# Kernel tuning notes

Measured on AMD Instinct MI355X. Metric: run time of the kernel, lower is better.

The kernel has to match this reference:

```python
import jax, jax.numpy as jnp
import numpy as np

BS, SEQ, H, L = 2, 4096, 768, 8921

def setup_inputs() -> dict:
    key = jax.random.key(0)
    k1, k2, k3 = jax.random.split(key, 3)
    return {
        "code_features": jax.random.normal(k1, (L, H), dtype=jnp.float32),
        "text_features": jax.random.normal(k2, (BS, SEQ, H), dtype=jnp.float32),
        "attention_mask": jnp.ones((BS, SEQ), dtype=jnp.int32),
        "W": jax.random.normal(k3, (H, H), dtype=jnp.float32) * (1.0 / np.sqrt(H)),
    }

def reference(code_features, text_features, attention_mask, W):
    # projected = tanh(Linear(text)) : (bs, seq, h)
    projected = jnp.tanh(jnp.einsum("bsh,kh->bsk", text_features, W))
    # scores: (bs, seq, labels); code_features broadcasts over batch
    scores = jnp.einsum("bsh,lh->bsl", projected, code_features)
    # softmax over the SEQ axis (dim=1), then transpose -> (bs, labels, seq)
    att_weights = jnp.transpose(jax.nn.softmax(scores, axis=1), (0, 2, 1))
    # weighted sum over seq -> (bs, labels, h)
    weighted_output = jnp.einsum("bls,bsh->blh", att_weights, text_features)
    return (att_weights, weighted_output)
```

## Files before the change

kernel.cpp:

```cpp
#include <hip/hip_runtime.h>
#include <math.h>

#define BSZ  2
#define SEQN 4096
#define HD   768
#define NL   8921

typedef _Float16 f16;
typedef f16   f16x8 __attribute__((ext_vector_type(8)));
typedef float f32x4 __attribute__((ext_vector_type(4)));

#define GPTR(p) ((const __attribute__((address_space(1))) void*)(p))
#define LPTR(p) ((__attribute__((address_space(3))) void*)(p))

__device__ __forceinline__ void stage_region(const f16* __restrict__ src, int ldk,
                                             int row0, int rowMax, int kbase,
                                             f16* region, int t)
{
    const int lane = t & 63, wv = t >> 6;
    #pragma unroll
    for (int qq = 0; qq < 2; ++qq) {
        const int base16 = wv * 64 + qq * 512;
        const int off16  = base16 + lane;
        const int row    = off16 >> 2;
        const int chunk  = off16 & 3;
        const int schunk = chunk ^ ((row >> 1) & 3);
        int grow = row0 + row; if (grow > rowMax) grow = rowMax;
        const f16* g = src + (long long)grow * ldk + kbase + schunk * 8;
        __builtin_amdgcn_global_load_lds(GPTR(g), LPTR(region + base16 * 8), 16, 0, 0);
    }
}

#define PH_SYNC_ENTER()                                          \
    __builtin_amdgcn_sched_barrier(0);                           \
    __builtin_amdgcn_s_barrier();                                \
    asm volatile("s_waitcnt lgkmcnt(0)" ::: "memory");           \
    __builtin_amdgcn_sched_barrier(0);                           \
    __builtin_amdgcn_s_setprio(1);

#define PH_SYNC_EXIT()                                           \
    __builtin_amdgcn_s_setprio(0);                               \
    __builtin_amdgcn_sched_barrier(0);                           \
    __builtin_amdgcn_s_barrier();

__global__ __launch_bounds__(512, 2)
void gemm8p(const f16* __restrict__ A, const f16* __restrict__ B,
            float* __restrict__ C, int M, int N, int K,
            long long sA, long long sB, long long sC, int ldA, int ldB)
{
    __shared__ __align__(16) f16 SH[2][2][2][256 * 32];

    const int t    = threadIdx.x;
    const int lane = t & 63;
    const int wv   = t >> 6;
    const int wm   = wv >> 2;
    const int wn   = wv & 3;
    const int rl   = lane & 15;
    const int swz8 = (((lane >> 4) ^ ((rl >> 1) & 3)) * 8);

    const int nx = gridDim.x, nwg = nx * gridDim.y;
    {
    }
    int orig = blockIdx.y * nx + blockIdx.x;
    const int q = nwg >> 3, r = nwg & 7, xcd = orig & 7, sub = orig >> 3;
    const int wg = (xcd < r ? xcd * (q + 1) : r * (q + 1) + (xcd - r) * q) + sub;
    const int bx = wg % nx, by = wg / nx;

    const f16* Ab = A + (long long)blockIdx.z * sA;
    const f16* Bb = B + (long long)blockIdx.z * sB;
    float*     Cb = C + (long long)blockIdx.z * sC;

    const int m0 = by * 256, n0 = bx * 256;
    const int NT = K >> 6;
    const int Mm1 = M - 1, Nm1 = N - 1;

    f32x4 acc[8][4];
    #pragma unroll
    for (int i = 0; i < 8; ++i)
        #pragma unroll
        for (int j = 0; j < 4; ++j)
            acc[i][j] = (f32x4)0.f;

    stage_region(Ab, ldA, m0, Mm1, 0,  &SH[0][0][0][0], t);
    stage_region(Bb, ldB, n0, Nm1, 0,  &SH[0][1][0][0], t);
    stage_region(Ab, ldA, m0, Mm1, 32, &SH[0][0][1][0], t);
    stage_region(Bb, ldB, n0, Nm1, 32, &SH[0][1][1][0], t);
    stage_region(Ab, ldA, m0, Mm1, 64, &SH[1][0][0][0], t);
    stage_region(Bb, ldB, n0, Nm1, 64, &SH[1][1][0][0], t);
    stage_region(Ab, ldA, m0, Mm1, 96, &SH[1][0][1][0], t);
    asm volatile("s_waitcnt vmcnt(6)" ::: "memory");
    __builtin_amdgcn_sched_barrier(0);
    __builtin_amdgcn_s_barrier();

    for (int tt = 0; tt < NT; ++tt) {
        const int buf = tt & 1;
        const f16* As0 = &SH[buf][0][0][0];
        const f16* As1 = &SH[buf][0][1][0];
        const f16* Bs0 = &SH[buf][1][0][0];
        const f16* Bs1 = &SH[buf][1][1][0];

        f16x8 af[8], bfa, bfb, bfc, bfd;

        #pragma unroll
        for (int f = 0; f < 8; ++f)
            af[f] = *(const f16x8*)&As0[(wm * 128 + f * 16 + rl) * 32 + swz8];
        bfa = *(const f16x8*)&Bs0[(wn * 64 + 0 * 16 + rl) * 32 + swz8];
        bfb = *(const f16x8*)&Bs0[(wn * 64 + 1 * 16 + rl) * 32 + swz8];
        if (tt + 1 < NT)
            stage_region(Bb, ldB, n0, Nm1, (tt + 1) * 64 + 32, &SH[buf ^ 1][1][1][0], t);
        PH_SYNC_ENTER();
        #pragma unroll
        for (int f = 0; f < 8; ++f) {
            acc[f][0] = __builtin_amdgcn_mfma_f32_16x16x32_f16(af[f], bfa, acc[f][0], 0, 0, 0);
            acc[f][1] = __builtin_amdgcn_mfma_f32_16x16x32_f16(af[f], bfb, acc[f][1], 0, 0, 0);
        }
        PH_SYNC_EXIT();

        bfc = *(const f16x8*)&Bs0[(wn * 64 + 2 * 16 + rl) * 32 + swz8];
        bfd = *(const f16x8*)&Bs0[(wn * 64 + 3 * 16 + rl) * 32 + swz8];
        if (tt + 2 < NT)
            stage_region(Ab, ldA, m0, Mm1, (tt + 2) * 64, &SH[buf][0][0][0], t);
        PH_SYNC_ENTER();
        #pragma unroll
        for (int f = 0; f < 8; ++f) {
            acc[f][2] = __builtin_amdgcn_mfma_f32_16x16x32_f16(af[f], bfc, acc[f][2], 0, 0, 0);
            acc[f][3] = __builtin_amdgcn_mfma_f32_16x16x32_f16(af[f], bfd, acc[f][3], 0, 0, 0);
        }
        PH_SYNC_EXIT();

        #pragma unroll
        for (int f = 0; f < 8; ++f)
            af[f] = *(const f16x8*)&As1[(wm * 128 + f * 16 + rl) * 32 + swz8];
        bfa = *(const f16x8*)&Bs1[(wn * 64 + 0 * 16 + rl) * 32 + swz8];
        bfb = *(const f16x8*)&Bs1[(wn * 64 + 1 * 16 + rl) * 32 + swz8];
        if (tt + 2 < NT)
            stage_region(Bb, ldB, n0, Nm1, (tt + 2) * 64, &SH[buf][1][0][0], t);
        PH_SYNC_ENTER();
        #pragma unroll
        for (int f = 0; f < 8; ++f) {
            acc[f][0] = __builtin_amdgcn_mfma_f32_16x16x32_f16(af[f], bfa, acc[f][0], 0, 0, 0);
            acc[f][1] = __builtin_amdgcn_mfma_f32_16x16x32_f16(af[f], bfb, acc[f][1], 0, 0, 0);
        }
        PH_SYNC_EXIT();

        bfc = *(const f16x8*)&Bs1[(wn * 64 + 2 * 16 + rl) * 32 + swz8];
        bfd = *(const f16x8*)&Bs1[(wn * 64 + 3 * 16 + rl) * 32 + swz8];
        if (tt + 2 < NT)
            stage_region(Ab, ldA, m0, Mm1, (tt + 2) * 64 + 32, &SH[buf][0][1][0], t);
        __builtin_amdgcn_sched_barrier(0);
        __builtin_amdgcn_s_barrier();
        asm volatile("s_waitcnt lgkmcnt(0)" ::: "memory");
        __builtin_amdgcn_sched_barrier(0);
        __builtin_amdgcn_s_setprio(1);
        #pragma unroll
        for (int f = 0; f < 8; ++f) {
            acc[f][2] = __builtin_amdgcn_mfma_f32_16x16x32_f16(af[f], bfc, acc[f][2], 0, 0, 0);
            acc[f][3] = __builtin_amdgcn_mfma_f32_16x16x32_f16(af[f], bfd, acc[f][3], 0, 0, 0);
        }
        __builtin_amdgcn_s_setprio(0);
        asm volatile("s_waitcnt vmcnt(6)" ::: "memory");
        __builtin_amdgcn_sched_barrier(0);
        __builtin_amdgcn_s_barrier();
    }

    const int rq = (lane >> 4) * 4;
    #pragma unroll
    for (int f = 0; f < 8; ++f) {
        #pragma unroll
        for (int j = 0; j < 4; ++j) {
            #pragma unroll
            for (int rr = 0; rr < 4; ++rr) {
                const int row = m0 + wm * 128 + f * 16 + rq + rr;
                const int col = n0 + wn * 64 + j * 16 + rl;
                if (row < M)
                    Cb[(long long)row * N + col] = acc[f][j][rr];
            }
        }
    }
}

template<int S16>
__device__ inline void stage_tile(const void* srcv, int ldk, int row0, int rowMax,
                                  int kt, f16* dst, int t, int lane, int wv)
{
    if constexpr (S16) {
        const f16* src = (const f16*)srcv;
        #pragma unroll
        for (int j = 0; j < 2; ++j) {
            int r = wv * 32 + j * 16 + (lane >> 2);
            int row = row0 + r; if (row > rowMax) row = rowMax;
            const f16* g = src + (long long)row * ldk + kt + (lane & 3) * 8;
            f16* l = dst + (wv * 32 + j * 16) * 32;
            __builtin_amdgcn_global_load_lds(GPTR(g), LPTR(l), 16, 0, 0);
        }
    } else {
        const float* src = (const float*)srcv;
        int r  = t >> 1;
        int kq = (t & 1) * 16;
        int row = row0 + r; if (row > rowMax) row = rowMax;
        const float* g = src + (long long)row * ldk + kt + kq;
        float4 v0 = ((const float4*)g)[0];
        float4 v1 = ((const float4*)g)[1];
        float4 v2 = ((const float4*)g)[2];
        float4 v3 = ((const float4*)g)[3];
        f16x8 h0, h1;
        h0[0]=(f16)v0.x; h0[1]=(f16)v0.y; h0[2]=(f16)v0.z; h0[3]=(f16)v0.w;
        h0[4]=(f16)v1.x; h0[5]=(f16)v1.y; h0[6]=(f16)v1.z; h0[7]=(f16)v1.w;
        h1[0]=(f16)v2.x; h1[1]=(f16)v2.y; h1[2]=(f16)v2.z; h1[3]=(f16)v2.w;
        h1[4]=(f16)v3.x; h1[5]=(f16)v3.y; h1[6]=(f16)v3.z; h1[7]=(f16)v3.w;
        *(f16x8*)&dst[r * 32 + kq]     = h0;
        *(f16x8*)&dst[r * 32 + kq + 8] = h1;
    }
}

template<int SA, int SB, int OUTMODE>
__global__ __launch_bounds__(256)
void mfma_nt(const void* __restrict__ A, const void* __restrict__ B,
             void* __restrict__ C, int M, int N, int K,
             long long sA, long long sB, long long sC, int ldA, int ldB)
{
    const char* Ab = (const char*)A + (long long)blockIdx.z * sA * (SA ? 2 : 4);
    const char* Bb = (const char*)B + (long long)blockIdx.z * sB * (SB ? 2 : 4);

    __shared__ __align__(16) f16 As[128 * 32];
    __shared__ __align__(16) f16 Bs[128 * 32];

    const int t    = threadIdx.x;
    const int lane = t & 63;
    const int wv   = t >> 6;
    const int wr   = wv >> 1;
    const int wc   = wv & 1;
    const int m0   = blockIdx.y * 128;
    const int n0   = blockIdx.x * 128;

    f32x4 acc[4][4] = {};

    for (int kt = 0; kt < K; kt += 32) {
        stage_tile<SA>(Ab, ldA, m0, M - 1, kt, As, t, lane, wv);
        stage_tile<SB>(Bb, ldB, n0, N - 1, kt, Bs, t, lane, wv);
        __syncthreads();

        f16x8 af[4], bf[4];
        const int kc = (lane >> 4) * 8;
        const int rl = lane & 15;
        #pragma unroll
        for (int i = 0; i < 4; ++i)
            af[i] = *(const f16x8*)&As[(wr * 64 + i * 16 + rl) * 32 + kc];
        #pragma unroll
        for (int j = 0; j < 4; ++j)
            bf[j] = *(const f16x8*)&Bs[(wc * 64 + j * 16 + rl) * 32 + kc];

        #pragma unroll
        for (int i = 0; i < 4; ++i)
            #pragma unroll
            for (int j = 0; j < 4; ++j)
                acc[i][j] = __builtin_amdgcn_mfma_f32_16x16x32_f16(af[i], bf[j], acc[i][j], 0, 0, 0);
        __syncthreads();
    }

    const int rquad = (lane >> 4) * 4;
    const int rcol  = lane & 15;
    #pragma unroll
    for (int i = 0; i < 4; ++i) {
        #pragma unroll
        for (int j = 0; j < 4; ++j) {
            #pragma unroll
            for (int r = 0; r < 4; ++r) {
                int row = m0 + wr * 64 + i * 16 + rquad + r;
                int col = n0 + wc * 64 + j * 16 + rcol;
                if (row < M) {
                    if constexpr (OUTMODE == 1)
                        ((f16*)C)[(long long)row * N + col] = (f16)tanhf(acc[i][j][r]);
                    else
                        ((float*)C + (long long)blockIdx.z * sC)[(long long)row * N + col] = acc[i][j][r];
                }
            }
        }
    }
}

__global__ __launch_bounds__(256)
void cvt_f32_f16(const float* __restrict__ in, f16* __restrict__ out, long long n4)
{
    long long i = (long long)blockIdx.x * 256 + threadIdx.x;
    if (i < n4) {
        float4 v = ((const float4*)in)[i];
        f16 h[4] = {(f16)v.x, (f16)v.y, (f16)v.z, (f16)v.w};
        *(uint2*)&out[i * 4] = *(uint2*)h;
    }
}

__global__ __launch_bounds__(256)
void transpose_f16(const float* __restrict__ in, f16* __restrict__ out)
{
    __shared__ float tile[32][33];
    const int b  = blockIdx.z;
    const int h0 = blockIdx.x * 32, s0 = blockIdx.y * 32;
    in  += (long long)b * SEQN * HD;
    out += (long long)b * HD * SEQN;
    const int tx = threadIdx.x & 31, ty = threadIdx.x >> 5;
    #pragma unroll
    for (int i = ty; i < 32; i += 8)
        tile[i][tx] = in[(long long)(s0 + i) * HD + h0 + tx];
    __syncthreads();
    #pragma unroll
    for (int i = ty; i < 32; i += 8)
        out[(long long)(h0 + i) * SEQN + s0 + tx] = (f16)tile[tx][i];
}

template<bool W16>
__global__ __launch_bounds__(256)
void softmax_rows(float* __restrict__ data, f16* __restrict__ data16)
{
    const long long row = blockIdx.x;
    float* p = data + row * (long long)SEQN;
    const int t = threadIdx.x;

    float4 v[4];
    float vmax = -INFINITY;
    #pragma unroll
    for (int i = 0; i < 4; ++i) {
        v[i] = ((const float4*)p)[t + 256 * i];
        vmax = fmaxf(vmax, fmaxf(fmaxf(v[i].x, v[i].y), fmaxf(v[i].z, v[i].w)));
    }
    #pragma unroll
    for (int off = 32; off > 0; off >>= 1)
        vmax = fmaxf(vmax, __shfl_xor(vmax, off));

    __shared__ float redmax[4];
    __shared__ float redsum[4];
    if ((t & 63) == 0) redmax[t >> 6] = vmax;
    __syncthreads();
    vmax = fmaxf(fmaxf(redmax[0], redmax[1]), fmaxf(redmax[2], redmax[3]));

    float sum = 0.f;
    #pragma unroll
    for (int i = 0; i < 4; ++i) {
        v[i].x = expf(v[i].x - vmax);
        v[i].y = expf(v[i].y - vmax);
        v[i].z = expf(v[i].z - vmax);
        v[i].w = expf(v[i].w - vmax);
        sum += (v[i].x + v[i].y) + (v[i].z + v[i].w);
    }
    #pragma unroll
    for (int off = 32; off > 0; off >>= 1)
        sum += __shfl_xor(sum, off);
    if ((t & 63) == 0) redsum[t >> 6] = sum;
    __syncthreads();
    sum = (redsum[0] + redsum[1]) + (redsum[2] + redsum[3]);

    const float inv = 1.0f / sum;
    #pragma unroll
    for (int i = 0; i < 4; ++i) {
        v[i].x *= inv; v[i].y *= inv; v[i].z *= inv; v[i].w *= inv;
        ((float4*)p)[t + 256 * i] = v[i];
        if constexpr (W16) {
            f16 h[4] = {(f16)v[i].x, (f16)v[i].y, (f16)v[i].z, (f16)v[i].w};
            *(uint2*)&data16[row * (long long)SEQN + (t + 256 * i) * 4] = *(uint2*)h;
        }
    }
}

#define BMF 64
#define BNF 64
#define BKF 16
#define PADF 4

template<bool TANH>
__global__ __launch_bounds__(256)
void nt_gemm(const float* __restrict__ A, const float* __restrict__ B,
             float* __restrict__ C, int M, int N, int K,
             long long sA, long long sB, long long sC)
{
    A += (long long)blockIdx.z * sA;
    B += (long long)blockIdx.z * sB;
    C += (long long)blockIdx.z * sC;
    __shared__ __align__(16) float As[BKF][BMF + PADF];
    __shared__ __align__(16) float Bs[BKF][BNF + PADF];
    const int t = threadIdx.x;
    const int m0 = blockIdx.y * BMF, n0 = blockIdx.x * BNF;
    const int tx = t & 15, ty = t >> 4, lr = t >> 2, lk = (t & 3) * 4;
    float acc[4][4] = {};
    for (int kt = 0; kt < K; kt += BKF) {
        {
            float4 v = make_float4(0.f, 0.f, 0.f, 0.f);
            int m = m0 + lr;
            if (m < M) v = *(const float4*)(A + (long long)m * K + kt + lk);
            As[lk+0][lr]=v.x; As[lk+1][lr]=v.y; As[lk+2][lr]=v.z; As[lk+3][lr]=v.w;
        }
        {
            float4 v = make_float4(0.f, 0.f, 0.f, 0.f);
            int n = n0 + lr;
            if (n < N) v = *(const float4*)(B + (long long)n * K + kt + lk);
            Bs[lk+0][lr]=v.x; Bs[lk+1][lr]=v.y; Bs[lk+2][lr]=v.z; Bs[lk+3][lr]=v.w;
        }
        __syncthreads();
        #pragma unroll
        for (int k = 0; k < BKF; ++k) {
            float4 a = *(const float4*)(&As[k][ty * 4]);
            float4 b = *(const float4*)(&Bs[k][tx * 4]);
            float av[4]={a.x,a.y,a.z,a.w}, bv[4]={b.x,b.y,b.z,b.w};
            #pragma unroll
            for (int i = 0; i < 4; ++i)
                #pragma unroll
                for (int j = 0; j < 4; ++j)
                    acc[i][j] = fmaf(av[i], bv[j], acc[i][j]);
        }
        __syncthreads();
    }
    #pragma unroll
    for (int i = 0; i < 4; ++i) {
        int m = m0 + ty * 4 + i;
        if (m < M) {
            float4 r;
            r.x = TANH ? tanhf(acc[i][0]) : acc[i][0];
            r.y = TANH ? tanhf(acc[i][1]) : acc[i][1];
            r.z = TANH ? tanhf(acc[i][2]) : acc[i][2];
            r.w = TANH ? tanhf(acc[i][3]) : acc[i][3];
            *(float4*)(C + (long long)m * N + n0 + tx * 4) = r;
        }
    }
}

__global__ __launch_bounds__(256)
void nn_gemm(const float* __restrict__ A, const float* __restrict__ B,
             float* __restrict__ C, int M, int N, int K,
             long long sA, long long sB, long long sC)
{
    A += (long long)blockIdx.z * sA;
    B += (long long)blockIdx.z * sB;
    C += (long long)blockIdx.z * sC;
    __shared__ __align__(16) float As[BKF][BMF + PADF];
    __shared__ __align__(16) float Bs[BKF][BNF + PADF];
    const int t = threadIdx.x;
    const int m0 = blockIdx.y * BMF, n0 = blockIdx.x * BNF;
    const int tx = t & 15, ty = t >> 4, lr = t >> 2, lk = (t & 3) * 4;
    const int kr = t >> 4, cq = (t & 15) * 4;
    float acc[4][4] = {};
    for (int kt = 0; kt < K; kt += BKF) {
        {
            float4 v = make_float4(0.f, 0.f, 0.f, 0.f);
            int m = m0 + lr;
            if (m < M) v = *(const float4*)(A + (long long)m * K + kt + lk);
            As[lk+0][lr]=v.x; As[lk+1][lr]=v.y; As[lk+2][lr]=v.z; As[lk+3][lr]=v.w;
        }
        {
            float4 v = *(const float4*)(B + (long long)(kt + kr) * N + n0 + cq);
            *(float4*)(&Bs[kr][cq]) = v;
        }
        __syncthreads();
        #pragma unroll
        for (int k = 0; k < BKF; ++k) {
            float4 a = *(const float4*)(&As[k][ty * 4]);
            float4 b = *(const float4*)(&Bs[k][tx * 4]);
            float av[4]={a.x,a.y,a.z,a.w}, bv[4]={b.x,b.y,b.z,b.w};
            #pragma unroll
            for (int i = 0; i < 4; ++i)
                #pragma unroll
                for (int j = 0; j < 4; ++j)
                    acc[i][j] = fmaf(av[i], bv[j], acc[i][j]);
        }
        __syncthreads();
    }
    #pragma unroll
    for (int i = 0; i < 4; ++i) {
        int m = m0 + ty * 4 + i;
        if (m < M)
            *(float4*)(C + (long long)m * N + n0 + tx * 4) =
                make_float4(acc[i][0], acc[i][1], acc[i][2], acc[i][3]);
    }
}

extern "C" void kernel_launch(void* const* d_in, const int* in_sizes, int n_in,
                              void* d_out, int out_size, void* d_ws, size_t ws_size,
                              hipStream_t stream)
{
    const float* code = (const float*)d_in[0];
    const float* text = (const float*)d_in[1];
    const float* Wm   = (const float*)d_in[3];

    float* att  = (float*)d_out;
    float* wout = att + (long long)BSZ * NL * SEQN;

    const long long n_code  = (long long)NL * HD;
    const long long n_proj  = (long long)BSZ * SEQN * HD;
    const long long n_textT = (long long)BSZ * HD * SEQN;
    const long long n_att   = (long long)BSZ * NL * SEQN;
    const size_t base_bytes = (size_t)(n_code + n_proj + n_textT) * 2;
    const size_t full_bytes = base_bytes + (size_t)n_att * 2;

    if (ws_size < base_bytes) {
        float* proj = wout;
        dim3 g1(HD / BNF, (BSZ * SEQN) / BMF, 1);
        hipLaunchKernelGGL((nt_gemm<true>), g1, dim3(256), 0, stream,
                           text, Wm, proj, BSZ * SEQN, HD, HD, 0LL, 0LL, 0LL);
        dim3 g2(SEQN / BNF, (NL + BMF - 1) / BMF, BSZ);
        hipLaunchKernelGGL((nt_gemm<false>), g2, dim3(256), 0, stream,
                           code, proj, att, NL, SEQN, HD,
                           0LL, (long long)SEQN * HD, (long long)NL * SEQN);
        hipLaunchKernelGGL((softmax_rows<false>), dim3(BSZ * NL), dim3(256), 0, stream, att, (f16*)nullptr);
        dim3 g4(HD / BNF, (NL + BMF - 1) / BMF, BSZ);
        hipLaunchKernelGGL(nn_gemm, g4, dim3(256), 0, stream,
                           att, text, wout, NL, HD, SEQN,
                           (long long)NL * SEQN, (long long)SEQN * HD, (long long)NL * HD);
        return;
    }

    f16* code_h  = (f16*)d_ws;
    f16* proj_h  = code_h + n_code;
    f16* textT_h = proj_h + n_proj;
    f16* att_h   = textT_h + n_textT;
    const bool has_att16 = ws_size >= full_bytes;

    {
        long long n4 = n_code / 4;
        hipLaunchKernelGGL(cvt_f32_f16, dim3((unsigned)((n4 + 255) / 256)), dim3(256), 0, stream,
                           code, code_h, n4);
    }
    {
        dim3 g(HD / 32, SEQN / 32, BSZ);
        hipLaunchKernelGGL(transpose_f16, g, dim3(256), 0, stream, text, textT_h);
    }
    {
        dim3 g(HD / 128, (BSZ * SEQN) / 128, 1);
        hipLaunchKernelGGL((mfma_nt<0, 0, 1>), g, dim3(256), 0, stream,
                           text, Wm, proj_h, BSZ * SEQN, HD, HD, 0LL, 0LL, 0LL, HD, HD);
    }
    {
        dim3 g(SEQN / 256, (NL + 255) / 256, BSZ);
        hipLaunchKernelGGL(gemm8p, g, dim3(512), 0, stream,
                           code_h, proj_h, att, NL, SEQN, HD,
                           0LL, (long long)SEQN * HD, (long long)NL * SEQN, HD, HD);
    }
    if (has_att16)
        hipLaunchKernelGGL((softmax_rows<true>), dim3(BSZ * NL), dim3(256), 0, stream, att, att_h);
    else
        hipLaunchKernelGGL((softmax_rows<false>), dim3(BSZ * NL), dim3(256), 0, stream, att, (f16*)nullptr);
    if (has_att16) {
        dim3 g(HD / 256, (NL + 255) / 256, BSZ);
        hipLaunchKernelGGL(gemm8p, g, dim3(512), 0, stream,
                           att_h, textT_h, wout, NL, HD, SEQN,
                           (long long)NL * SEQN, (long long)HD * SEQN, (long long)NL * HD,
                           SEQN, SEQN);
    } else {
        dim3 g(HD / 128, (NL + 127) / 128, BSZ);
        hipLaunchKernelGGL((mfma_nt<0, 1, 0>), g, dim3(256), 0, stream,
                           att, textT_h, wout, NL, HD, SEQN,
                           (long long)NL * SEQN, (long long)HD * SEQN, (long long)NL * HD,
                           SEQN, SEQN);
    }
}
```

Before: 481.8 us.

## Store GEMM scores as fp16 and run softmax in place on fp16 buffer

```diff
diff --git a/kernel.cpp b/kernel.cpp
--- a/kernel.cpp
+++ b/kernel.cpp
@@ -43,9 +43,10 @@
     __builtin_amdgcn_sched_barrier(0);                           \
     __builtin_amdgcn_s_barrier();
 
+template<int OUT>
 __global__ __launch_bounds__(512, 2)
 void gemm8p(const f16* __restrict__ A, const f16* __restrict__ B,
-            float* __restrict__ C, int M, int N, int K,
+            void* __restrict__ C, int M, int N, int K,
             long long sA, long long sB, long long sC, int ldA, int ldB)
 {
     __shared__ __align__(16) f16 SH[2][2][2][256 * 32];
@@ -59,8 +60,6 @@
     const int swz8 = (((lane >> 4) ^ ((rl >> 1) & 3)) * 8);
 
     const int nx = gridDim.x, nwg = nx * gridDim.y;
-    {
-    }
     int orig = blockIdx.y * nx + blockIdx.x;
     const int q = nwg >> 3, r = nwg & 7, xcd = orig & 7, sub = orig >> 3;
     const int wg = (xcd < r ? xcd * (q + 1) : r * (q + 1) + (xcd - r) * q) + sub;
@@ -68,7 +67,6 @@
 
     const f16* Ab = A + (long long)blockIdx.z * sA;
     const f16* Bb = B + (long long)blockIdx.z * sB;
-    float*     Cb = C + (long long)blockIdx.z * sC;
 
     const int m0 = by * 256, n0 = bx * 256;
     const int NT = K >> 6;
@@ -172,8 +170,12 @@
             for (int rr = 0; rr < 4; ++rr) {
                 const int row = m0 + wm * 128 + f * 16 + rq + rr;
                 const int col = n0 + wn * 64 + j * 16 + rl;
-                if (row < M)
-                    Cb[(long long)row * N + col] = acc[f][j][rr];
+                if (row < M) {
+                    if constexpr (OUT == 1)
+                        ((f16*)C + (long long)blockIdx.z * sC)[(long long)row * N + col] = (f16)acc[f][j][rr];
+                    else
+                        ((float*)C + (long long)blockIdx.z * sC)[(long long)row * N + col] = acc[f][j][rr];
+                }
             }
         }
     }
@@ -308,20 +310,25 @@
         out[(long long)(h0 + i) * SEQN + s0 + tx] = (f16)tile[tx][i];
 }
 
-template<bool W16>
-__global__ __launch_bounds__(256)
-void softmax_rows(float* __restrict__ data, f16* __restrict__ data16)
+__global__ __launch_bounds__(256)
+void softmax_f16(f16* __restrict__ scores, float* __restrict__ att)
 {
     const long long row = blockIdx.x;
-    float* p = data + row * (long long)SEQN;
+    f16*   ps = scores + row * (long long)SEQN;
+    float* pa = att    + row * (long long)SEQN;
     const int t = threadIdx.x;
 
-    float4 v[4];
+    f16x8 h[2];
+    float x[2][8];
     float vmax = -INFINITY;
     #pragma unroll
-    for (int i = 0; i < 4; ++i) {
-        v[i] = ((const float4*)p)[t + 256 * i];
-        vmax = fmaxf(vmax, fmaxf(fmaxf(v[i].x, v[i].y), fmaxf(v[i].z, v[i].w)));
+    for (int i = 0; i < 2; ++i) {
+        h[i] = ((const f16x8*)ps)[t + 256 * i];
+        #pragma unroll
+        for (int j = 0; j < 8; ++j) {
+            x[i][j] = (float)h[i][j];
+            vmax = fmaxf(vmax, x[i][j]);
+        }
     }
     #pragma unroll
     for (int off = 32; off > 0; off >>= 1)
@@ -335,13 +342,12 @@
 
     float sum = 0.f;
     #pragma unroll
-    for (int i = 0; i < 4; ++i) {
-        v[i].x = expf(v[i].x - vmax);
-        v[i].y = expf(v[i].y - vmax);
-        v[i].z = expf(v[i].z - vmax);
-        v[i].w = expf(v[i].w - vmax);
-        sum += (v[i].x + v[i].y) + (v[i].z + v[i].w);
-    }
+    for (int i = 0; i < 2; ++i)
+        #pragma unroll
+        for (int j = 0; j < 8; ++j) {
+            x[i][j] = expf(x[i][j] - vmax);
+            sum += x[i][j];
+        }
     #pragma unroll
     for (int off = 32; off > 0; off >>= 1)
         sum += __shfl_xor(sum, off);
@@ -351,13 +357,18 @@
 
     const float inv = 1.0f / sum;
     #pragma unroll
-    for (int i = 0; i < 4; ++i) {
-        v[i].x *= inv; v[i].y *= inv; v[i].z *= inv; v[i].w *= inv;
-        ((float4*)p)[t + 256 * i] = v[i];
-        if constexpr (W16) {
-            f16 h[4] = {(f16)v[i].x, (f16)v[i].y, (f16)v[i].z, (f16)v[i].w};
-            *(uint2*)&data16[row * (long long)SEQN + (t + 256 * i) * 4] = *(uint2*)h;
-        }
+    for (int i = 0; i < 2; ++i) {
+        f16x8 hn;
+        #pragma unroll
+        for (int j = 0; j < 8; ++j) {
+            x[i][j] *= inv;
+            hn[j] = (f16)x[i][j];
+        }
+        float4 lo = make_float4(x[i][0], x[i][1], x[i][2], x[i][3]);
+        float4 hi = make_float4(x[i][4], x[i][5], x[i][6], x[i][7]);
+        ((float4*)pa)[(t + 256 * i) * 2 + 0] = lo;
+        ((float4*)pa)[(t + 256 * i) * 2 + 1] = hi;
+        ((f16x8*)ps)[t + 256 * i] = hn;
     }
 }
 
@@ -365,6 +376,48 @@
 #define BNF 64
 #define BKF 16
 #define PADF 4
+
+__global__ __launch_bounds__(256)
+void softmax_rows_f32(float* __restrict__ data)
+{
+    const long long row = blockIdx.x;
+    float* p = data + row * (long long)SEQN;
+    const int t = threadIdx.x;
+    float4 v[4];
+    float vmax = -INFINITY;
+    #pragma unroll
+    for (int i = 0; i < 4; ++i) {
+        v[i] = ((const float4*)p)[t + 256 * i];
+        vmax = fmaxf(vmax, fmaxf(fmaxf(v[i].x, v[i].y), fmaxf(v[i].z, v[i].w)));
+    }
+    #pragma unroll
+    for (int off = 32; off > 0; off >>= 1)
+        vmax = fmaxf(vmax, __shfl_xor(vmax, off));
+    __shared__ float redmax[4];
+    __shared__ float redsum[4];
+    if ((t & 63) == 0) redmax[t >> 6] = vmax;
+    __syncthreads();
+    vmax = fmaxf(fmaxf(redmax[0], redmax[1]), fmaxf(redmax[2], redmax[3]));
+    float sum = 0.f;
+    #pragma unroll
+    for (int i = 0; i < 4; ++i) {
+        v[i].x = expf(v[i].x - vmax); v[i].y = expf(v[i].y - vmax);
+        v[i].z = expf(v[i].z - vmax); v[i].w = expf(v[i].w - vmax);
+        sum += (v[i].x + v[i].y) + (v[i].z + v[i].w);
+    }
+    #pragma unroll
+    for (int off = 32; off > 0; off >>= 1)
+        sum += __shfl_xor(sum, off);
+    if ((t & 63) == 0) redsum[t >> 6] = sum;
+    __syncthreads();
+    sum = (redsum[0] + redsum[1]) + (redsum[2] + redsum[3]);
+    const float inv = 1.0f / sum;
+    #pragma unroll
+    for (int i = 0; i < 4; ++i) {
+        v[i].x *= inv; v[i].y *= inv; v[i].z *= inv; v[i].w *= inv;
+        ((float4*)p)[t + 256 * i] = v[i];
+    }
+}
 
 template<bool TANH>
 __global__ __launch_bounds__(256)
@@ -486,10 +539,9 @@
     const long long n_proj  = (long long)BSZ * SEQN * HD;
     const long long n_textT = (long long)BSZ * HD * SEQN;
     const long long n_att   = (long long)BSZ * NL * SEQN;
-    const size_t base_bytes = (size_t)(n_code + n_proj + n_textT) * 2;
-    const size_t full_bytes = base_bytes + (size_t)n_att * 2;
-
-    if (ws_size < base_bytes) {
+    const size_t need_bytes = (size_t)(n_code + n_proj + n_textT + n_att) * 2;
+
+    if (ws_size < need_bytes) {
         float* proj = wout;
         dim3 g1(HD / BNF, (BSZ * SEQN) / BMF, 1);
         hipLaunchKernelGGL((nt_gemm<true>), g1, dim3(256), 0, stream,
@@ -498,7 +550,7 @@
         hipLaunchKernelGGL((nt_gemm<false>), g2, dim3(256), 0, stream,
                            code, proj, att, NL, SEQN, HD,
                            0LL, (long long)SEQN * HD, (long long)NL * SEQN);
-        hipLaunchKernelGGL((softmax_rows<false>), dim3(BSZ * NL), dim3(256), 0, stream, att, (f16*)nullptr);
+        hipLaunchKernelGGL(softmax_rows_f32, dim3(BSZ * NL), dim3(256), 0, stream, att);
         dim3 g4(HD / BNF, (NL + BMF - 1) / BMF, BSZ);
         hipLaunchKernelGGL(nn_gemm, g4, dim3(256), 0, stream,
                            att, text, wout, NL, HD, SEQN,
@@ -506,11 +558,10 @@
         return;
     }
 
-    f16* code_h  = (f16*)d_ws;
-    f16* proj_h  = code_h + n_code;
-    f16* textT_h = proj_h + n_proj;
-    f16* att_h   = textT_h + n_textT;
-    const bool has_att16 = ws_size >= full_bytes;
+    f16* code_h   = (f16*)d_ws;
+    f16* proj_h   = code_h + n_code;
+    f16* textT_h  = proj_h + n_proj;
+    f16* scores_h = textT_h + n_textT;
 
     {
         long long n4 = n_code / 4;
@@ -528,25 +579,16 @@
     }
     {
         dim3 g(SEQN / 256, (NL + 255) / 256, BSZ);
-        hipLaunchKernelGGL(gemm8p, g, dim3(512), 0, stream,
-                           code_h, proj_h, att, NL, SEQN, HD,
+        hipLaunchKernelGGL((gemm8p<1>), g, dim3(512), 0, stream,
+                           code_h, proj_h, scores_h, NL, SEQN, HD,
                            0LL, (long long)SEQN * HD, (long long)NL * SEQN, HD, HD);
     }
-    if (has_att16)
-        hipLaunchKernelGGL((softmax_rows<true>), dim3(BSZ * NL), dim3(256), 0, stream, att, att_h);
-    else
-        hipLaunchKernelGGL((softmax_rows<false>), dim3(BSZ * NL), dim3(256), 0, stream, att, (f16*)nullptr);
-    if (has_att16) {
+    hipLaunchKernelGGL(softmax_f16, dim3(BSZ * NL), dim3(256), 0, stream, scores_h, att);
+    {
         dim3 g(HD / 256, (NL + 255) / 256, BSZ);
-        hipLaunchKernelGGL(gemm8p, g, dim3(512), 0, stream,
-                           att_h, textT_h, wout, NL, HD, SEQN,
+        hipLaunchKernelGGL((gemm8p<0>), g, dim3(512), 0, stream,
+                           scores_h, textT_h, wout, NL, HD, SEQN,
                            (long long)NL * SEQN, (long long)HD * SEQN, (long long)NL * HD,
                            SEQN, SEQN);
-    } else {
-        dim3 g(HD / 128, (NL + 127) / 128, BSZ);
-        hipLaunchKernelGGL((mfma_nt<0, 1, 0>), g, dim3(256), 0, stream,
-                           att, textT_h, wout, NL, HD, SEQN,
-                           (long long)NL * SEQN, (long long)HD * SEQN, (long long)NL * HD,
-                           SEQN, SEQN);
-    }
-}
+    }
+}
```

New measurement: 419.6 us, median of 2. 1.15x faster.
